# Kernel tuning notes

Hardware: AMD Instinct MI355X
Metric: run time of the kernel (lower is better)

The kernel has to match this reference:

```python
import jax, jax.numpy as jnp
import numpy as np

N_NODES = 20000
N_EDGES = 320000
HIDDEN = 256
N_GRAPHS = 64
IN_DIM = 3
OUT_DIM = 2


def _glorot(key, shape):
    fan_in, fan_out = shape
    lim = jnp.sqrt(6.0 / (fan_in + fan_out))
    return jax.random.uniform(key, shape, jnp.float32, -lim, lim)


def setup_inputs() -> dict:
    key = jax.random.key(0)
    ks = jax.random.split(key, 16)
    inp = {
        "x": jax.random.normal(ks[0], (N_NODES, IN_DIM), jnp.float32),
        "edge_index": jax.random.randint(ks[1], (2, N_EDGES), 0, N_NODES, jnp.int64),
        "batch": jnp.sort(jax.random.randint(ks[2], (N_NODES,), 0, N_GRAPHS, jnp.int64)),
        "W1": _glorot(ks[3], (IN_DIM, HIDDEN)), "b1": jnp.zeros((HIDDEN,), jnp.float32),
        "W2": _glorot(ks[4], (HIDDEN, HIDDEN)), "b2": jnp.zeros((HIDDEN,), jnp.float32),
        "W3": _glorot(ks[5], (HIDDEN, HIDDEN)), "b3": jnp.zeros((HIDDEN,), jnp.float32),
        "W4": _glorot(ks[6], (HIDDEN, HIDDEN)), "b4": jnp.zeros((HIDDEN,), jnp.float32),
        "W5": _glorot(ks[7], (HIDDEN, HIDDEN)), "b5": jnp.zeros((HIDDEN,), jnp.float32),
        "Wlin": _glorot(ks[8], (HIDDEN, OUT_DIM)), "blin": jnp.zeros((OUT_DIM,), jnp.float32),
    }
    return inp


def _gcn_norm(edge_index, n_nodes):
    # PyG GCNConv default: add self-loops, symmetric degree normalization.
    loops = jnp.arange(n_nodes, dtype=edge_index.dtype)
    src = jnp.concatenate([edge_index[0], loops])
    dst = jnp.concatenate([edge_index[1], loops])
    deg = jax.ops.segment_sum(jnp.ones_like(dst, jnp.float32), dst, num_segments=n_nodes)
    dinv = jnp.where(deg > 0, jax.lax.rsqrt(deg), 0.0)
    norm = dinv[src] * dinv[dst]  # [E + N]
    return src, dst, norm


def _gcn_layer(x, W, b, src, dst, norm, n_nodes):
    h = x @ W                                   # [N, H]
    msg = h[src] * norm[:, None]                # [E+N, H] gather + scale
    agg = jax.ops.segment_sum(msg, dst, num_segments=n_nodes)  # scatter-add
    return agg + b


def reference(x, edge_index, batch, W1, b1, W2, b2, W3, b3, W4, b4, W5, b5, Wlin, blin):
    n = x.shape[0]
    src, dst, norm = _gcn_norm(edge_index, n)
    h = jax.nn.relu(_gcn_layer(x, W1, b1, src, dst, norm, n))
    h = jax.nn.relu(_gcn_layer(h, W2, b2, src, dst, norm, n))
    h = jax.nn.relu(_gcn_layer(h, W3, b3, src, dst, norm, n))
    h = jax.nn.relu(_gcn_layer(h, W4, b4, src, dst, norm, n))
    h = jax.nn.relu(_gcn_layer(h, W5, b5, src, dst, norm, n))
    pooled = jax.ops.segment_sum(h, batch, num_segments=N_GRAPHS)  # global_add_pool
    return pooled @ Wlin + blin
```

## Files before the change

### kernel.cpp

```cpp
#include <hip/hip_runtime.h>

#define N_NODES 20000
#define N_PAD 20032
#define N_EDGES 320000
#define HIDDEN 256
#define N_GRAPHS 64
#define OUT_DIM 2

#define QPANEL_BYTES 65536
#define QTABLE_BYTES 32768

typedef __attribute__((ext_vector_type(8))) short short8v;
typedef __attribute__((ext_vector_type(4))) float f32x4;
typedef __attribute__((ext_vector_type(4))) unsigned short us4;

__global__ void k_degree(const int* __restrict__ dst, int* __restrict__ degi) {
    int e = blockIdx.x * blockDim.x + threadIdx.x;
    if (e < N_EDGES) atomicAdd(&degi[dst[e]], 1);
}

__global__ void k_scan(const int* __restrict__ degi, int* __restrict__ rowptr,
                       int* __restrict__ rowstart, float* __restrict__ dinv) {
    __shared__ int sums[1024];
    int t = threadIdx.x;
    int base = t * 20;
    int ld[20];
    int local = 0;
    if (t < 1000) {
#pragma unroll
        for (int i = 0; i < 20; ++i) {
            ld[i] = degi[base + i];
            local += ld[i];
            dinv[base + i] = rsqrtf((float)ld[i] + 1.0f);
        }
    }
    sums[t] = local;
    __syncthreads();
    for (int off = 1; off < 1024; off <<= 1) {
        int v = (t >= off) ? sums[t - off] : 0;
        __syncthreads();
        sums[t] += v;
        __syncthreads();
    }
    if (t < 1000) {
        int run = (t == 0) ? 0 : sums[t - 1];
#pragma unroll
        for (int i = 0; i < 20; ++i) {
            rowptr[base + i] = run;
            rowstart[base + i] = run;
            run += ld[i];
        }
    }
    if (t == 1023) rowptr[N_NODES] = sums[1023];
}

__global__ void k_fill(const int* __restrict__ src, const int* __restrict__ dst,
                       const float* __restrict__ dinv, int* __restrict__ rowstart,
                       int2* __restrict__ csr) {
    int e = blockIdx.x * blockDim.x + threadIdx.x;
    if (e >= N_EDGES) return;
    int s = src[e], d = dst[e];
    int pos = atomicAdd(&rowstart[d], 1);
    csr[pos] = make_int2(s, __float_as_int(dinv[s] * dinv[d]));
}

__global__ void k_wprep4(const float* __restrict__ W2, const float* __restrict__ W3,
                         const float* __restrict__ W4, const float* __restrict__ W5,
                         char* __restrict__ wt) {
    int lid = blockIdx.x >> 8;
    int idx = (blockIdx.x & 255) * 256 + threadIdx.x;
    const float* W = lid == 0 ? W2 : lid == 1 ? W3 : lid == 2 ? W4 : W5;
    int k = idx & 255, n = idx >> 8;
    float a = W[k * 256 + n];
    unsigned u = __float_as_uint(a);
    ushort hi = (ushort)(u >> 16);
    float hif = __uint_as_float(u & 0xffff0000u);
    ushort lo = (ushort)(__float_as_uint(a - hif) >> 16);
    int q = n >> 6, colQ = n & 63, slab = k >> 3, e = k & 7;
    size_t base = ((size_t)lid * 4 + q) * QPANEL_BYTES;
    size_t soff = (size_t)slab * 1024 + ((colQ * 16 + slab * 32) & 1023) + e * 2;
    *(ushort*)(wt + base + soff) = hi;
    *(ushort*)(wt + base + QTABLE_BYTES + soff) = lo;
}

__global__ void k_aggx(const float* __restrict__ x, const float* __restrict__ dinv,
                       const int* __restrict__ rowptr, const int2* __restrict__ csr,
                       float* __restrict__ z) {
    int t = blockIdx.x * blockDim.x + threadIdx.x;
    int i = t >> 2, c = t & 3;
    if (i >= N_NODES || c >= 3) return;
    float di = dinv[i];
    float a = di * di * x[i * 3 + c], bacc = 0.f;
    int k = rowptr[i], end = rowptr[i + 1];
    for (; k + 1 < end; k += 2) {
        int2 e0 = csr[k], e1 = csr[k + 1];
        a = fmaf(x[(size_t)e0.x * 3 + c], __int_as_float(e0.y), a);
        bacc = fmaf(x[(size_t)e1.x * 3 + c], __int_as_float(e1.y), bacc);
    }
    if (k < end) {
        int2 e0 = csr[k];
        a = fmaf(x[(size_t)e0.x * 3 + c], __int_as_float(e0.y), a);
    }
    z[i * 3 + c] = a + bacc;
}

__global__ void k_h1(const float* __restrict__ z, const float* __restrict__ W1,
                     const float* __restrict__ b1,
                     ushort* __restrict__ out_hi, ushort* __restrict__ out_lo) {
    int i = blockIdx.x;
    int j = threadIdx.x;
    float z0 = z[i * 3], z1 = z[i * 3 + 1], z2 = z[i * 3 + 2];
    float v = fmaf(z0, W1[j], fmaf(z1, W1[256 + j], fmaf(z2, W1[512 + j], b1[j])));
    v = fmaxf(v, 0.0f);
    unsigned u = __float_as_uint(v);
    ushort hi = (ushort)(u >> 16);
    float hif = __uint_as_float(u & 0xffff0000u);
    ushort lo = (ushort)(__float_as_uint(v - hif) >> 16);
    out_hi[(size_t)i * HIDDEN + j] = hi;
    out_lo[(size_t)i * HIDDEN + j] = lo;
}

__global__ void k_csr_agg(const float* __restrict__ h, const float* __restrict__ dinv,
                          const int* __restrict__ rowptr, const int2* __restrict__ csr,
                          const float* __restrict__ b,
                          ushort* __restrict__ out_hi, ushort* __restrict__ out_lo) {
    int node = blockIdx.x * 4 + (threadIdx.x >> 6);
    if (node >= N_NODES) return;
    int lane = threadIdx.x & 63;
    int beg = rowptr[node], end = rowptr[node + 1];
    float di = dinv[node];
    float w0 = di * di;
    float4 bv = *reinterpret_cast<const float4*>(b + lane * 4);
    float4 hv = *reinterpret_cast<const float4*>(h + (size_t)node * HIDDEN + lane * 4);
    float4 A0, A1 = {0,0,0,0}, A2 = {0,0,0,0}, A3 = {0,0,0,0};
    A0.x = fmaf(hv.x, w0, bv.x);
    A0.y = fmaf(hv.y, w0, bv.y);
    A0.z = fmaf(hv.z, w0, bv.z);
    A0.w = fmaf(hv.w, w0, bv.w);
    int k = beg;
    for (; k + 3 < end; k += 4) {
        int2 e0 = csr[k], e1 = csr[k + 1], e2 = csr[k + 2], e3 = csr[k + 3];
        float we0 = __int_as_float(e0.y), we1 = __int_as_float(e1.y);
        float we2 = __int_as_float(e2.y), we3 = __int_as_float(e3.y);
        float4 v0 = *reinterpret_cast<const float4*>(h + (size_t)e0.x * HIDDEN + lane * 4);
        float4 v1 = *reinterpret_cast<const float4*>(h + (size_t)e1.x * HIDDEN + lane * 4);
        float4 v2 = *reinterpret_cast<const float4*>(h + (size_t)e2.x * HIDDEN + lane * 4);
        float4 v3 = *reinterpret_cast<const float4*>(h + (size_t)e3.x * HIDDEN + lane * 4);
        A0.x = fmaf(v0.x, we0, A0.x);  A1.x = fmaf(v1.x, we1, A1.x);
        A0.y = fmaf(v0.y, we0, A0.y);  A1.y = fmaf(v1.y, we1, A1.y);
        A0.z = fmaf(v0.z, we0, A0.z);  A1.z = fmaf(v1.z, we1, A1.z);
        A0.w = fmaf(v0.w, we0, A0.w);  A1.w = fmaf(v1.w, we1, A1.w);
        A2.x = fmaf(v2.x, we2, A2.x);  A3.x = fmaf(v3.x, we3, A3.x);
        A2.y = fmaf(v2.y, we2, A2.y);  A3.y = fmaf(v3.y, we3, A3.y);
        A2.z = fmaf(v2.z, we2, A2.z);  A3.z = fmaf(v3.z, we3, A3.z);
        A2.w = fmaf(v2.w, we2, A2.w);  A3.w = fmaf(v3.w, we3, A3.w);
    }
    for (; k < end; ++k) {
        int2 e0 = csr[k];
        float we0 = __int_as_float(e0.y);
        float4 v0 = *reinterpret_cast<const float4*>(h + (size_t)e0.x * HIDDEN + lane * 4);
        A0.x = fmaf(v0.x, we0, A0.x);
        A0.y = fmaf(v0.y, we0, A0.y);
        A0.z = fmaf(v0.z, we0, A0.z);
        A0.w = fmaf(v0.w, we0, A0.w);
    }
    float4 acc;
    acc.x = (A0.x + A1.x) + (A2.x + A3.x);
    acc.y = (A0.y + A1.y) + (A2.y + A3.y);
    acc.z = (A0.z + A1.z) + (A2.z + A3.z);
    acc.w = (A0.w + A1.w) + (A2.w + A3.w);
    float rv[4] = {fmaxf(acc.x, 0.f), fmaxf(acc.y, 0.f), fmaxf(acc.z, 0.f), fmaxf(acc.w, 0.f)};
    us4 hvv, lvv;
#pragma unroll
    for (int j = 0; j < 4; ++j) {
        unsigned u = __float_as_uint(rv[j]);
        hvv[j] = (ushort)(u >> 16);
        float hif = __uint_as_float(u & 0xffff0000u);
        lvv[j] = (ushort)(__float_as_uint(rv[j] - hif) >> 16);
    }
    *reinterpret_cast<us4*>(out_hi + (size_t)node * HIDDEN + lane * 4) = hvv;
    *reinterpret_cast<us4*>(out_lo + (size_t)node * HIDDEN + lane * 4) = lvv;
}

__global__ __launch_bounds__(256) void k_gemm_mfma(const ushort* __restrict__ a_hi,
                                                   const ushort* __restrict__ a_lo,
                                                   const char* __restrict__ wpanels,
                                                   float* __restrict__ out) {
    __shared__ char smem[QPANEL_BYTES];
    int bx = blockIdx.x;
    int q = bx & 3;
    int mtile = bx >> 2;
    const char* gsrc = wpanels + (size_t)q * QPANEL_BYTES;
    int tid = threadIdx.x;
#pragma unroll
    for (int it = 0; it < 16; ++it) {
        int o = it * 4096 + tid * 16;
        *reinterpret_cast<float4*>(smem + o) = *reinterpret_cast<const float4*>(gsrc + o);
    }
    __syncthreads();

    int w = tid >> 6, l = tid & 63;
    int lr = l & 15, kg = l >> 4;
    int wm = w >> 1, wn = w & 1;
    int row0 = mtile * 64 + wm * 32;
    int colQ0 = wn * 32;

    const ushort* aph = a_hi + (size_t)(row0 + lr) * HIDDEN + kg * 8;
    const ushort* apl = a_lo + (size_t)(row0 + lr) * HIDDEN + kg * 8;

    f32x4 acc[2][2] = {};
#pragma unroll
    for (int t = 0; t < 8; ++t) {
        int kb = t * 32;
        short8v ah0 = *reinterpret_cast<const short8v*>(aph + kb);
        short8v ah1 = *reinterpret_cast<const short8v*>(aph + 16 * HIDDEN + kb);
        short8v al0 = *reinterpret_cast<const short8v*>(apl + kb);
        short8v al1 = *reinterpret_cast<const short8v*>(apl + 16 * HIDDEN + kb);
        int slab = t * 4 + kg;
        int sbase = slab * 1024;
        int rot = slab * 32;
        int off0 = sbase + (((colQ0 + lr) * 16 + rot) & 1023);
        int off1 = sbase + (((colQ0 + 16 + lr) * 16 + rot) & 1023);
        short8v bh0 = *reinterpret_cast<const short8v*>(smem + off0);
        short8v bh1 = *reinterpret_cast<const short8v*>(smem + off1);
        short8v bl0 = *reinterpret_cast<const short8v*>(smem + QTABLE_BYTES + off0);
        short8v bl1 = *reinterpret_cast<const short8v*>(smem + QTABLE_BYTES + off1);
        acc[0][0] = __builtin_amdgcn_mfma_f32_16x16x32_bf16(ah0, bh0, acc[0][0], 0, 0, 0);
        acc[1][0] = __builtin_amdgcn_mfma_f32_16x16x32_bf16(ah1, bh0, acc[1][0], 0, 0, 0);
        acc[0][1] = __builtin_amdgcn_mfma_f32_16x16x32_bf16(ah0, bh1, acc[0][1], 0, 0, 0);
        acc[1][1] = __builtin_amdgcn_mfma_f32_16x16x32_bf16(ah1, bh1, acc[1][1], 0, 0, 0);
        acc[0][0] = __builtin_amdgcn_mfma_f32_16x16x32_bf16(al0, bh0, acc[0][0], 0, 0, 0);
        acc[1][0] = __builtin_amdgcn_mfma_f32_16x16x32_bf16(al1, bh0, acc[1][0], 0, 0, 0);
        acc[0][1] = __builtin_amdgcn_mfma_f32_16x16x32_bf16(al0, bh1, acc[0][1], 0, 0, 0);
        acc[1][1] = __builtin_amdgcn_mfma_f32_16x16x32_bf16(al1, bh1, acc[1][1], 0, 0, 0);
        acc[0][0] = __builtin_amdgcn_mfma_f32_16x16x32_bf16(ah0, bl0, acc[0][0], 0, 0, 0);
        acc[1][0] = __builtin_amdgcn_mfma_f32_16x16x32_bf16(ah1, bl0, acc[1][0], 0, 0, 0);
        acc[0][1] = __builtin_amdgcn_mfma_f32_16x16x32_bf16(ah0, bl1, acc[0][1], 0, 0, 0);
        acc[1][1] = __builtin_amdgcn_mfma_f32_16x16x32_bf16(ah1, bl1, acc[1][1], 0, 0, 0);
    }
    int gcol = q * 64 + colQ0 + lr;
#pragma unroll
    for (int rf = 0; rf < 2; ++rf) {
        float* o0 = out + (size_t)(row0 + rf * 16 + kg * 4) * HIDDEN + gcol;
#pragma unroll
        for (int r = 0; r < 4; ++r)
#pragma unroll
            for (int cf = 0; cf < 2; ++cf)
                o0[(size_t)r * HIDDEN + cf * 16] = acc[rf][cf][r];
    }
}

__global__ void k_pool(const ushort* __restrict__ hi, const ushort* __restrict__ lo,
                       const int* __restrict__ batch, float* __restrict__ pooled) {
    int base = blockIdx.x * 32;
    int j = threadIdx.x;
    float acc = 0.0f;
    int cur = batch[base];
    for (int r = 0; r < 32; ++r) {
        int i = base + r;
        int bg = batch[i];
        if (bg != cur) {
            atomicAdd(&pooled[cur * HIDDEN + j], acc);
            acc = 0.0f;
            cur = bg;
        }
        size_t off = (size_t)i * HIDDEN + j;
        float v = __uint_as_float((unsigned)hi[off] << 16) +
                  __uint_as_float((unsigned)lo[off] << 16);
        acc += v;
    }
    atomicAdd(&pooled[cur * HIDDEN + j], acc);
}

__global__ void k_final(const float* __restrict__ pooled, const float* __restrict__ Wlin,
                        const float* __restrict__ blin, float* __restrict__ out) {
    int t = threadIdx.x;
    int g = t >> 1, o = t & 1;
    float s = blin[o];
    for (int k = 0; k < HIDDEN; ++k) s += pooled[g * HIDDEN + k] * Wlin[k * OUT_DIM + o];
    out[g * OUT_DIM + o] = s;
}

extern "C" void kernel_launch(void* const* d_in, const int* in_sizes, int n_in,
                              void* d_out, int out_size, void* d_ws, size_t ws_size,
                              hipStream_t stream) {
    const float* x     = (const float*)d_in[0];
    const int*   esrc  = (const int*)d_in[1];
    const int*   edst  = esrc + N_EDGES;
    const int*   batch = (const int*)d_in[2];
    const float* W1 = (const float*)d_in[3];
    const float* b1 = (const float*)d_in[4];
    const float* W2 = (const float*)d_in[5];
    const float* b2 = (const float*)d_in[6];
    const float* W3 = (const float*)d_in[7];
    const float* b3 = (const float*)d_in[8];
    const float* W4 = (const float*)d_in[9];
    const float* b4 = (const float*)d_in[10];
    const float* W5 = (const float*)d_in[11];
    const float* b5 = (const float*)d_in[12];
    const float* Wlin = (const float*)d_in[13];
    const float* blin = (const float*)d_in[14];
    float* out = (float*)d_out;

    char* ws = (char*)d_ws;
    size_t off = 0;
    auto alloc = [&](size_t bytes) { size_t o = off; off += (bytes + 255) & ~size_t(255); return (void*)(ws + o); };

    int*    degi     = (int*)alloc(N_NODES * 4);
    float*  dinv     = (float*)alloc(N_NODES * 4);
    int*    rowptr   = (int*)alloc((N_NODES + 1) * 4);
    int*    rowstart = (int*)alloc(N_NODES * 4);
    int2*   csr      = (int2*)alloc((size_t)N_EDGES * 8);
    float*  hA       = (float*)alloc((size_t)N_PAD * HIDDEN * 4);
    ushort* hb_hi    = (ushort*)alloc((size_t)N_PAD * HIDDEN * 2);
    ushort* hb_lo    = (ushort*)alloc((size_t)N_PAD * HIDDEN * 2);
    float*  pooled   = (float*)alloc(N_GRAPHS * HIDDEN * 4);
    char*   wt       = (char*)alloc((size_t)4 * 4 * QPANEL_BYTES);
    float*  z        = (float*)alloc((size_t)N_NODES * 3 * 4);

    hipMemsetAsync(degi, 0, N_NODES * 4, stream);
    hipMemsetAsync(pooled, 0, N_GRAPHS * HIDDEN * 4, stream);

    k_degree<<<(N_EDGES + 255) / 256, 256, 0, stream>>>(edst, degi);
    k_scan<<<1, 1024, 0, stream>>>(degi, rowptr, rowstart, dinv);
    k_fill<<<(N_EDGES + 255) / 256, 256, 0, stream>>>(esrc, edst, dinv, rowstart, csr);
    k_wprep4<<<1024, 256, 0, stream>>>(W2, W3, W4, W5, wt);

    const float* bs[5] = {b1, b2, b3, b4, b5};

    k_aggx<<<(N_NODES * 4 + 255) / 256, 256, 0, stream>>>(x, dinv, rowptr, csr, z);
    k_h1<<<N_NODES, HIDDEN, 0, stream>>>(z, W1, b1, hb_hi, hb_lo);

    for (int l = 1; l < 5; ++l) {
        k_gemm_mfma<<<313 * 4, 256, 0, stream>>>(
            hb_hi, hb_lo, wt + (size_t)(l - 1) * 4 * QPANEL_BYTES, hA);
        k_csr_agg<<<N_NODES / 4, 256, 0, stream>>>(hA, dinv, rowptr, csr, bs[l], hb_hi, hb_lo);
    }

    k_pool<<<N_NODES / 32, HIDDEN, 0, stream>>>(hb_hi, hb_lo, batch, pooled);
    k_final<<<1, 128, 0, stream>>>(pooled, Wlin, blin, out);
}
```

Baseline: 392.2 us.

## Double GEMM block size, add XCD-aware block remap and A-operand prefetch

The MFMA GEMM now runs 512-thread blocks that each cover 128 rows, so each block's 64KB weight-panel load into LDS is amortized over twice as many rows, and the grid is halved to 628. Block IDs are remapped so consecutive logical tiles land on the same XCD, which should improve L2 locality. The A-operand global loads are software-pipelined one k-step ahead to overlap load latency with MFMA work. N_PAD grows to cover the larger row tiles. The cost is more registers per thread and fewer blocks in flight.

```diff
diff --git a/kernel.cpp b/kernel.cpp
--- a/kernel.cpp
+++ b/kernel.cpp
@@ -1,7 +1,7 @@
 #include <hip/hip_runtime.h>
 
 #define N_NODES 20000
-#define N_PAD 20032
+#define N_PAD 20096
 #define N_EDGES 320000
 #define HIDDEN 256
 #define N_GRAPHS 64
@@ -9,6 +9,7 @@
 
 #define QPANEL_BYTES 65536
 #define QTABLE_BYTES 32768
+#define GEMM_GRID 628
 
 typedef __attribute__((ext_vector_type(8))) short short8v;
 typedef __attribute__((ext_vector_type(4))) float f32x4;
@@ -182,19 +183,23 @@
     *reinterpret_cast<us4*>(out_lo + (size_t)node * HIDDEN + lane * 4) = lvv;
 }
 
-__global__ __launch_bounds__(256) void k_gemm_mfma(const ushort* __restrict__ a_hi,
+__global__ __launch_bounds__(512) void k_gemm_mfma(const ushort* __restrict__ a_hi,
                                                    const ushort* __restrict__ a_lo,
                                                    const char* __restrict__ wpanels,
                                                    float* __restrict__ out) {
     __shared__ char smem[QPANEL_BYTES];
-    int bx = blockIdx.x;
-    int q = bx & 3;
-    int mtile = bx >> 2;
+    int d = blockIdx.x;
+    int xcd = d & 7, idx = d >> 3;
+    const int q0 = GEMM_GRID / 8, r = GEMM_GRID % 8;
+    int base = xcd * q0 + (xcd < r ? xcd : r);
+    int logical = base + idx;
+    int mtile = logical >> 2, q = logical & 3;
+
     const char* gsrc = wpanels + (size_t)q * QPANEL_BYTES;
     int tid = threadIdx.x;
 #pragma unroll
-    for (int it = 0; it < 16; ++it) {
-        int o = it * 4096 + tid * 16;
+    for (int it = 0; it < 8; ++it) {
+        int o = it * 8192 + tid * 16;
         *reinterpret_cast<float4*>(smem + o) = *reinterpret_cast<const float4*>(gsrc + o);
     }
     __syncthreads();
@@ -202,20 +207,28 @@
     int w = tid >> 6, l = tid & 63;
     int lr = l & 15, kg = l >> 4;
     int wm = w >> 1, wn = w & 1;
-    int row0 = mtile * 64 + wm * 32;
+    int row0 = mtile * 128 + wm * 32;
     int colQ0 = wn * 32;
 
     const ushort* aph = a_hi + (size_t)(row0 + lr) * HIDDEN + kg * 8;
     const ushort* apl = a_lo + (size_t)(row0 + lr) * HIDDEN + kg * 8;
 
+    short8v ah0 = *reinterpret_cast<const short8v*>(aph);
+    short8v ah1 = *reinterpret_cast<const short8v*>(aph + 16 * HIDDEN);
+    short8v al0 = *reinterpret_cast<const short8v*>(apl);
+    short8v al1 = *reinterpret_cast<const short8v*>(apl + 16 * HIDDEN);
+
     f32x4 acc[2][2] = {};
 #pragma unroll
     for (int t = 0; t < 8; ++t) {
-        int kb = t * 32;
-        short8v ah0 = *reinterpret_cast<const short8v*>(aph + kb);
-        short8v ah1 = *reinterpret_cast<const short8v*>(aph + 16 * HIDDEN + kb);
-        short8v al0 = *reinterpret_cast<const short8v*>(apl + kb);
-        short8v al1 = *reinterpret_cast<const short8v*>(apl + 16 * HIDDEN + kb);
+        short8v cah0 = ah0, cah1 = ah1, cal0 = al0, cal1 = al1;
+        if (t < 7) {
+            int kb = (t + 1) * 32;
+            ah0 = *reinterpret_cast<const short8v*>(aph + kb);
+            ah1 = *reinterpret_cast<const short8v*>(aph + 16 * HIDDEN + kb);
+            al0 = *reinterpret_cast<const short8v*>(apl + kb);
+            al1 = *reinterpret_cast<const short8v*>(apl + 16 * HIDDEN + kb);
+        }
         int slab = t * 4 + kg;
         int sbase = slab * 1024;
         int rot = slab * 32;
@@ -225,28 +238,28 @@
         short8v bh1 = *reinterpret_cast<const short8v*>(smem + off1);
         short8v bl0 = *reinterpret_cast<const short8v*>(smem + QTABLE_BYTES + off0);
         short8v bl1 = *reinterpret_cast<const short8v*>(smem + QTABLE_BYTES + off1);
-        acc[0][0] = __builtin_amdgcn_mfma_f32_16x16x32_bf16(ah0, bh0, acc[0][0], 0, 0, 0);
-        acc[1][0] = __builtin_amdgcn_mfma_f32_16x16x32_bf16(ah1, bh0, acc[1][0], 0, 0, 0);
-        acc[0][1] = __builtin_amdgcn_mfma_f32_16x16x32_bf16(ah0, bh1, acc[0][1], 0, 0, 0);
-        acc[1][1] = __builtin_amdgcn_mfma_f32_16x16x32_bf16(ah1, bh1, acc[1][1], 0, 0, 0);
-        acc[0][0] = __builtin_amdgcn_mfma_f32_16x16x32_bf16(al0, bh0, acc[0][0], 0, 0, 0);
-        acc[1][0] = __builtin_amdgcn_mfma_f32_16x16x32_bf16(al1, bh0, acc[1][0], 0, 0, 0);
-        acc[0][1] = __builtin_amdgcn_mfma_f32_16x16x32_bf16(al0, bh1, acc[0][1], 0, 0, 0);
-        acc[1][1] = __builtin_amdgcn_mfma_f32_16x16x32_bf16(al1, bh1, acc[1][1], 0, 0, 0);
-        acc[0][0] = __builtin_amdgcn_mfma_f32_16x16x32_bf16(ah0, bl0, acc[0][0], 0, 0, 0);
-        acc[1][0] = __builtin_amdgcn_mfma_f32_16x16x32_bf16(ah1, bl0, acc[1][0], 0, 0, 0);
-        acc[0][1] = __builtin_amdgcn_mfma_f32_16x16x32_bf16(ah0, bl1, acc[0][1], 0, 0, 0);
-        acc[1][1] = __builtin_amdgcn_mfma_f32_16x16x32_bf16(ah1, bl1, acc[1][1], 0, 0, 0);
+        acc[0][0] = __builtin_amdgcn_mfma_f32_16x16x32_bf16(cah0, bh0, acc[0][0], 0, 0, 0);
+        acc[1][0] = __builtin_amdgcn_mfma_f32_16x16x32_bf16(cah1, bh0, acc[1][0], 0, 0, 0);
+        acc[0][1] = __builtin_amdgcn_mfma_f32_16x16x32_bf16(cah0, bh1, acc[0][1], 0, 0, 0);
+        acc[1][1] = __builtin_amdgcn_mfma_f32_16x16x32_bf16(cah1, bh1, acc[1][1], 0, 0, 0);
+        acc[0][0] = __builtin_amdgcn_mfma_f32_16x16x32_bf16(cal0, bh0, acc[0][0], 0, 0, 0);
+        acc[1][0] = __builtin_amdgcn_mfma_f32_16x16x32_bf16(cal1, bh0, acc[1][0], 0, 0, 0);
+        acc[0][1] = __builtin_amdgcn_mfma_f32_16x16x32_bf16(cal0, bh1, acc[0][1], 0, 0, 0);
+        acc[1][1] = __builtin_amdgcn_mfma_f32_16x16x32_bf16(cal1, bh1, acc[1][1], 0, 0, 0);
+        acc[0][0] = __builtin_amdgcn_mfma_f32_16x16x32_bf16(cah0, bl0, acc[0][0], 0, 0, 0);
+        acc[1][0] = __builtin_amdgcn_mfma_f32_16x16x32_bf16(cah1, bl0, acc[1][0], 0, 0, 0);
+        acc[0][1] = __builtin_amdgcn_mfma_f32_16x16x32_bf16(cah0, bl1, acc[0][1], 0, 0, 0);
+        acc[1][1] = __builtin_amdgcn_mfma_f32_16x16x32_bf16(cah1, bl1, acc[1][1], 0, 0, 0);
     }
     int gcol = q * 64 + colQ0 + lr;
 #pragma unroll
     for (int rf = 0; rf < 2; ++rf) {
         float* o0 = out + (size_t)(row0 + rf * 16 + kg * 4) * HIDDEN + gcol;
 #pragma unroll
-        for (int r = 0; r < 4; ++r)
+        for (int rr = 0; rr < 4; ++rr)
 #pragma unroll
             for (int cf = 0; cf < 2; ++cf)
-                o0[(size_t)r * HIDDEN + cf * 16] = acc[rf][cf][r];
+                o0[(size_t)rr * HIDDEN + cf * 16] = acc[rf][cf][rr];
     }
 }
 
@@ -332,7 +345,7 @@
     k_h1<<<N_NODES, HIDDEN, 0, stream>>>(z, W1, b1, hb_hi, hb_lo);
 
     for (int l = 1; l < 5; ++l) {
-        k_gemm_mfma<<<313 * 4, 256, 0, stream>>>(
+        k_gemm_mfma<<<GEMM_GRID, 512, 0, stream>>>(
             hb_hi, hb_lo, wt + (size_t)(l - 1) * 4 * QPANEL_BYTES, hA);
         k_csr_agg<<<N_NODES / 4, 256, 0, stream>>>(hA, dinv, rowptr, csr, bs[l], hb_hi, hb_lo);
     }
```

New measurement: 385.9 us. Within noise of the previous version (-1.6%).
